# Performance work log

Hardware: AMD Instinct MI355X
Metric: run time of the kernel (lower is better)

Reference implementation:

```python
import jax, jax.numpy as jnp
import numpy as np

B, N = 256, 4096
IMG_W, IMG_H = 640.0, 480.0


def setup_inputs() -> dict:
    key = jax.random.key(0)
    k0, k1, k2, k3 = jax.random.split(key, 4)
    kpts0 = jax.random.uniform(k0, (B, N, 2), dtype=jnp.float32) * jnp.array([IMG_W, IMG_H], jnp.float32)
    kpts1 = jax.random.uniform(k1, (B, N, 2), dtype=jnp.float32) * jnp.array([IMG_W, IMG_H], jnp.float32)
    conf = jax.random.uniform(k2, (B, N, 1), dtype=jnp.float32)
    t_scale = jax.random.uniform(k3, (B, 2), dtype=jnp.float32) + 0.5
    Kmat = jnp.array([[500.0, 0.0, 320.0], [0.0, 500.0, 240.0], [0.0, 0.0, 1.0]], jnp.float32)
    K = jnp.tile(Kmat[None, None], (B, 2, 1, 1))
    gt_pose_0to1 = jnp.tile(jnp.eye(4, dtype=jnp.float32)[None], (B, 1, 1))
    return {"kpts0": kpts0, "kpts1": kpts1, "conf": conf, "t_scale": t_scale, "K": K, "gt_pose_0to1": gt_pose_0to1}


def _normalize(kpts, Kmat):
    # pixel -> normalized camera coords, homogeneous. kpts:[B,N,2], Kmat:[B,3,3] -> [B,N,3]
    Kinv = jnp.linalg.inv(Kmat)
    h = jnp.concatenate([kpts, jnp.ones_like(kpts[..., :1])], axis=-1)
    return jnp.einsum('bij,bnj->bni', Kinv, h)


def _se3_weighted_8pt(kpts0, kpts1, K0, K1, w, t_scale):
    b_, n_ = kpts0.shape[0], kpts0.shape[1]
    x0 = _normalize(kpts0, K0)  # [B,N,3]
    x1 = _normalize(kpts1, K1)  # [B,N,3]
    # epipolar constraint x1^T E x0 = 0 -> row kron(x1, x0): [B,N,9]
    X = (x1[..., :, None] * x0[..., None, :]).reshape(b_, n_, 9)
    # confidence-weighted normal equations, 9x9 per batch
    M = jnp.einsum('bn,bni,bnj->bij', w, X, X)
    _, V = jnp.linalg.eigh(M)
    E = V[..., 0].reshape(b_, 3, 3)  # eigvec of smallest eigenvalue
    # project to essential manifold + decompose
    U, S, Vt = jnp.linalg.svd(E)
    W = jnp.array([[0.0, -1.0, 0.0], [1.0, 0.0, 0.0], [0.0, 0.0, 1.0]], E.dtype)
    R1 = U @ W @ Vt
    R2 = U @ W.T @ Vt
    R1 = R1 * jnp.sign(jnp.linalg.det(R1))[:, None, None]
    R2 = R2 * jnp.sign(jnp.linalg.det(R2))[:, None, None]
    t = U[..., 2]  # [B,3]
    Rc = jnp.stack([R1, R1, R2, R2], axis=1)   # [B,4,3,3]
    tc = jnp.stack([t, -t, t, -t], axis=1)     # [B,4,3]
    # cheirality: solve d0 * (R x0) - d1 * x1 = -t in least squares (2x2 closed form)
    a = jnp.einsum('bcij,bnj->bcni', Rc, x0)   # [B,4,N,3]
    bvec = x1[:, None]                          # [B,1,N,3]
    tt = tc[:, :, None, :]                      # [B,4,1,3]
    aa = jnp.sum(a * a, -1)
    bb = jnp.sum(bvec * bvec, -1)
    ab = jnp.sum(a * bvec, -1)
    at = jnp.sum(a * tt, -1)
    bt = jnp.sum(bvec * tt, -1)
    det = aa * bb - ab * ab + 1e-9
    d0 = (-at * bb + ab * bt) / det
    d1 = (aa * bt - ab * at) / det
    pos = ((d0 > 0) & (d1 > 0)).astype(w.dtype)
    score = jnp.sum(w[:, None] * pos, -1)       # [B,4]
    best = jnp.argmax(jax.lax.stop_gradient(score), axis=-1)
    oh = jax.nn.one_hot(best, 4, dtype=kpts0.dtype)
    R = jnp.einsum('bc,bcij->bij', oh, Rc)
    t_best = jnp.einsum('bc,bci->bi', oh, tc)
    t_sc = t_best * t_scale[:, None]            # scale unit translation
    top = jnp.concatenate([R, t_sc[..., None]], axis=-1)  # [B,3,4]
    bot = jnp.broadcast_to(jnp.array([0.0, 0.0, 0.0, 1.0], R.dtype), (b_, 1, 4))
    return jnp.concatenate([top, bot], axis=1)  # [B,4,4]


def _se3_inverse(T):
    R = T[:, :3, :3]
    t = T[:, :3, 3:]
    Rt = jnp.swapaxes(R, -1, -2)
    tin = -(Rt @ t)
    top = jnp.concatenate([Rt, tin], axis=-1)
    bot = jnp.broadcast_to(jnp.array([0.0, 0.0, 0.0, 1.0], T.dtype), (T.shape[0], 1, 4))
    return jnp.concatenate([top, bot], axis=1)


def reference(kpts0, kpts1, conf, t_scale, K, gt_pose_0to1):
    w = conf[..., 0]
    T01 = _se3_weighted_8pt(kpts0, kpts1, K[:, 0], K[:, 1], w, t_scale[:, 0])
    T10 = _se3_inverse(T01)
    return jnp.stack([T01, T10], axis=1)  # [B,2,4,4]
```

## Files before the change

### kernel.cpp

```cpp
#include <hip/hip_runtime.h>
#include <math.h>

#define NBATCH 256
#define NPTS   4096
#define NT     512
#define PPT    (NPTS / NT)
#define NWAVE  (NT / 64)

#define IDX(r,c)   ((r)*((r)+1)/2+(c))
#define UPIDX(r,c) ((r)*9 - ((r)*((r)-1))/2 + ((c)-(r)))

__device__ __forceinline__ void inv3x3f(const float* __restrict__ Km, float* Ki) {
  double a = Km[0], bb = Km[1], c = Km[2];
  double d = Km[3], e  = Km[4], f = Km[5];
  double g = Km[6], h  = Km[7], i = Km[8];
  double C00 =  e*i - f*h;
  double C01 = -(d*i - f*g);
  double C02 =  d*h - e*g;
  double det = a*C00 + bb*C01 + c*C02;
  double rd = 1.0/det;
  Ki[0] = (float)(C00*rd); Ki[1] = (float)(-(bb*i - c*h)*rd); Ki[2] = (float)( (bb*f - c*e)*rd);
  Ki[3] = (float)(C01*rd); Ki[4] = (float)( (a*i  - c*g)*rd); Ki[5] = (float)(-(a*f  - c*d)*rd);
  Ki[6] = (float)(C02*rd); Ki[7] = (float)(-(a*h - bb*g)*rd); Ki[8] = (float)( (a*e  - bb*d)*rd);
}

__global__ __launch_bounds__(NT, 1)
void pose_fused(const float* __restrict__ kpts0,
                const float* __restrict__ kpts1,
                const float* __restrict__ conf,
                const float* __restrict__ t_scale,
                const float* __restrict__ Kmat,
                float* __restrict__ out)
{
  const int b    = blockIdx.x;
  const int tid  = threadIdx.x;
  const int lane = tid & 63;
  const int wv   = tid >> 6;

  __shared__ float  red[NWAVE][45];
  __shared__ double sMd[45];
  __shared__ double sLp[45];
  __shared__ double sDinv[9];
  __shared__ double sW[81];
  __shared__ double sB[81];
  __shared__ float  sR[21];
  __shared__ float  sscore[NWAVE][4];

  float Ki0[9], Ki1[9];
  inv3x3f(Kmat + (size_t)b*18,     Ki0);
  inv3x3f(Kmat + (size_t)b*18 + 9, Ki1);

  const float4* k0p4 = (const float4*)(kpts0 + (size_t)b*NPTS*2);
  const float4* k1p4 = (const float4*)(kpts1 + (size_t)b*NPTS*2);
  const float2* cp2  = (const float2*)(conf  + (size_t)b*NPTS);

  float px0[PPT][3], px1[PPT][3], pw[PPT];
  float acc[45];
#pragma unroll
  for (int j=0;j<45;j++) acc[j] = 0.f;

#pragma unroll
  for (int p=0;p<PPT/2;p++) {
    const int idx = tid + p*NT;
    const float4 q0 = k0p4[idx];
    const float4 q1 = k1p4[idx];
    const float2 w2 = cp2[idx];
#pragma unroll
    for (int h=0; h<2; h++) {
      const int pt = 2*p + h;
      const float u0 = h ? q0.z : q0.x, v0 = h ? q0.w : q0.y;
      const float u1 = h ? q1.z : q1.x, v1 = h ? q1.w : q1.y;
      const float w  = h ? w2.y : w2.x;
      float x0[3], x1[3];
      x0[0] = fmaf(Ki0[0],u0, fmaf(Ki0[1],v0, Ki0[2]));
      x0[1] = fmaf(Ki0[3],u0, fmaf(Ki0[4],v0, Ki0[5]));
      x0[2] = fmaf(Ki0[6],u0, fmaf(Ki0[7],v0, Ki0[8]));
      x1[0] = fmaf(Ki1[0],u1, fmaf(Ki1[1],v1, Ki1[2]));
      x1[1] = fmaf(Ki1[3],u1, fmaf(Ki1[4],v1, Ki1[5]));
      x1[2] = fmaf(Ki1[6],u1, fmaf(Ki1[7],v1, Ki1[8]));
#pragma unroll
      for (int j=0;j<3;j++) { px0[pt][j] = x0[j]; px1[pt][j] = x1[j]; }
      pw[pt] = w;
      float X[9], wX[9];
#pragma unroll
      for (int ii=0; ii<3; ii++)
#pragma unroll
        for (int jj=0; jj<3; jj++)
          X[ii*3+jj] = x1[ii]*x0[jj];
#pragma unroll
      for (int j=0;j<9;j++) wX[j] = w*X[j];
      int k = 0;
#pragma unroll
      for (int r=0;r<9;r++)
#pragma unroll
        for (int c=r;c<9;c++) { acc[k] = fmaf(wX[r], X[c], acc[k]); k++; }
    }
  }

#pragma unroll
  for (int j=0;j<45;j++) {
    float v = acc[j];
#pragma unroll
    for (int off=32; off>0; off>>=1) v += __shfl_xor(v, off, 64);
    acc[j] = v;
  }
  if (lane == 0) {
#pragma unroll
    for (int j=0;j<45;j++) red[wv][j] = acc[j];
  }
  __syncthreads();
  if (tid < 45) {
    double s = 0.0;
#pragma unroll
    for (int wq=0; wq<NWAVE; wq++) s += (double)red[wq][tid];
    sMd[tid] = s;
  }
  __syncthreads();

  if (wv == 0) {
    if (lane == 0) {
      double L[45];
#pragma unroll
      for (int r=0;r<9;r++)
#pragma unroll
        for (int c=0;c<=r;c++)
          L[IDX(r,c)] = sMd[UPIDX(c,r)];

      double dinv[9];
#pragma unroll
      for (int k=0;k<9;k++) {
        double s = L[IDX(k,k)];
#pragma unroll
        for (int j=0;j<k;j++) s -= L[IDX(k,j)]*L[IDX(k,j)];
        double l = sqrt(fmax(s, 1e-30));
        L[IDX(k,k)] = l;
        dinv[k] = 1.0/l;
#pragma unroll
        for (int i2=k+1;i2<9;i2++) {
          double s2 = L[IDX(i2,k)];
#pragma unroll
          for (int j=0;j<k;j++) s2 -= L[IDX(i2,j)]*L[IDX(k,j)];
          L[IDX(i2,k)] = s2*dinv[k];
        }
      }
#pragma unroll
      for (int j=0;j<45;j++) sLp[j] = L[j];
#pragma unroll
      for (int k=0;k<9;k++) sDinv[k] = dinv[k];
    }
    asm volatile("s_waitcnt lgkmcnt(0)" ::: "memory");
    __builtin_amdgcn_sched_barrier(0);

    double Brow[9];
    double vlan[9];
    if (lane < 9) {
      const double dj = sDinv[lane];
      double cw[9];
#pragma unroll
      for (int i=0;i<9;i++) cw[i] = (i == lane) ? dj : 0.0;
#pragma unroll
      for (int i2=1;i2<9;i2++) {
        double s = 0.0;
#pragma unroll
        for (int k=0;k<i2;k++) s = fma(sLp[IDX(i2,k)], cw[k], s);
        const double ci2 = -s*sDinv[i2];
        cw[i2] = (i2 > lane) ? ci2 : cw[i2];
      }
#pragma unroll
      for (int k=0;k<9;k++) sW[k*9 + lane] = cw[k];
    }
    asm volatile("s_waitcnt lgkmcnt(0)" ::: "memory");
    __builtin_amdgcn_sched_barrier(0);

    if (lane < 9) {
      double wcol[9];
#pragma unroll
      for (int k=0;k<9;k++) wcol[k] = sW[k*9 + lane];
#pragma unroll
      for (int j=0;j<9;j++) {
        double s = 0.0;
#pragma unroll
        for (int k=0;k<9;k++) s = fma(wcol[k], sW[k*9 + j], s);
        Brow[j] = s;
      }
#pragma unroll
      for (int j=0;j<9;j++) sB[lane*9 + j] = Brow[j];
    }
    asm volatile("s_waitcnt lgkmcnt(0)" ::: "memory");
    __builtin_amdgcn_sched_barrier(0);

    if (lane < 9) {
      double Crow[9];
#pragma unroll
      for (int j=0;j<9;j++) {
        double s = 0.0;
#pragma unroll
        for (int k=0;k<9;k++) s = fma(Brow[k], sB[k*9 + j], s);
        Crow[j] = s;
      }

      double vv[9];
#pragma unroll
      for (int j=0;j<9;j++) vv[j] = 0.125;
      vv[4] = 1.0;
      for (int it=0; it<10; ++it) {
        double p0 = fma(Crow[1], vv[1], Crow[0]*vv[0]);
        double p1 = fma(Crow[3], vv[3], Crow[2]*vv[2]);
        double p2 = fma(Crow[5], vv[5], Crow[4]*vv[4]);
        double p3 = fma(Crow[7], vv[7], Crow[6]*vv[6]);
        double p4 = Crow[8]*vv[8];
        double y  = ((p0 + p1) + (p2 + p3)) + p4;
#pragma unroll
        for (int j=0;j<9;j++) vv[j] = __shfl(y, j, 64);
      }
#pragma unroll
      for (int j=0;j<9;j++) vlan[j] = vv[j];
    }

    if (lane == 0) {
      double v[9];
#pragma unroll
      for (int j=0;j<9;j++) v[j] = vlan[j];
      {
        double nn = 0.0;
#pragma unroll
        for (int j=0;j<9;j++) nn += v[j]*v[j];
        double rn = 1.0/sqrt(nn);
#pragma unroll
        for (int j=0;j<9;j++) v[j] *= rn;
      }

      double E0[3][3];
#pragma unroll
      for (int ii=0;ii<3;ii++)
#pragma unroll
        for (int jj=0;jj<3;jj++) E0[ii][jj] = v[ii*3+jj];
      double G[3][3];
#pragma unroll
      for (int a2=0;a2<3;a2++)
#pragma unroll
        for (int b2=0;b2<3;b2++)
          G[a2][b2] = E0[0][a2]*E0[0][b2] + E0[1][a2]*E0[1][b2] + E0[2][a2]*E0[2][b2];
      double Vv[3][3] = {{1,0,0},{0,1,0},{0,0,1}};
#define JROT(P,Q,RR) do { \
      double apq = G[P][Q]; \
      if (fabs(apq) > 1e-18*(fabs(G[P][P])+fabs(G[Q][Q]))) { \
        double app = G[P][P], aqq = G[Q][Q]; \
        double tau = (aqq - app) / (2.0*apq); \
        double tt = ((tau >= 0.0) ? 1.0 : -1.0) / (fabs(tau) + sqrt(1.0 + tau*tau)); \
        double cc_ = 1.0/sqrt(1.0 + tt*tt); \
        double ss_ = tt*cc_; \
        G[P][P] = app - tt*apq; \
        G[Q][Q] = aqq + tt*apq; \
        G[P][Q] = 0.0; G[Q][P] = 0.0; \
        double grp = G[RR][P], grq = G[RR][Q]; \
        G[RR][P] = cc_*grp - ss_*grq; G[P][RR] = G[RR][P]; \
        G[RR][Q] = ss_*grp + cc_*grq; G[Q][RR] = G[RR][Q]; \
        double v0p = Vv[0][P], v0q = Vv[0][Q]; \
        Vv[0][P] = cc_*v0p - ss_*v0q; Vv[0][Q] = ss_*v0p + cc_*v0q; \
        double v1p = Vv[1][P], v1q = Vv[1][Q]; \
        Vv[1][P] = cc_*v1p - ss_*v1q; Vv[1][Q] = ss_*v1p + cc_*v1q; \
        double v2p = Vv[2][P], v2q = Vv[2][Q]; \
        Vv[2][P] = cc_*v2p - ss_*v2q; Vv[2][Q] = ss_*v2p + cc_*v2q; \
      } } while(0)
      for (int sw=0; sw<6; sw++) { JROT(0,1,2); JROT(0,2,1); JROT(1,2,0); }
#undef JROT
      double lam[3] = {G[0][0], G[1][1], G[2][2]};
#define CSWAP(A_,B_) if (lam[A_] < lam[B_]) { \
      double tl = lam[A_]; lam[A_] = lam[B_]; lam[B_] = tl; \
      double t0_ = Vv[0][A_]; Vv[0][A_] = Vv[0][B_]; Vv[0][B_] = t0_; \
      double t1_ = Vv[1][A_]; Vv[1][A_] = Vv[1][B_]; Vv[1][B_] = t1_; \
      double t2_ = Vv[2][A_]; Vv[2][A_] = Vv[2][B_]; Vv[2][B_] = t2_; }
      CSWAP(0,1); CSWAP(0,2); CSWAP(1,2);
#undef CSWAP
      double u1[3], u2[3], u3[3];
#pragma unroll
      for (int i3=0;i3<3;i3++)
        u1[i3] = E0[i3][0]*Vv[0][0] + E0[i3][1]*Vv[1][0] + E0[i3][2]*Vv[2][0];
      double n1 = 1.0/sqrt(fmax(u1[0]*u1[0]+u1[1]*u1[1]+u1[2]*u1[2], 1e-300));
#pragma unroll
      for (int i3=0;i3<3;i3++) u1[i3] *= n1;
#pragma unroll
      for (int i3=0;i3<3;i3++)
        u2[i3] = E0[i3][0]*Vv[0][1] + E0[i3][1]*Vv[1][1] + E0[i3][2]*Vv[2][1];
      double d12 = u1[0]*u2[0]+u1[1]*u2[1]+u1[2]*u2[2];
#pragma unroll
      for (int i3=0;i3<3;i3++) u2[i3] -= d12*u1[i3];
      double n2 = 1.0/sqrt(fmax(u2[0]*u2[0]+u2[1]*u2[1]+u2[2]*u2[2], 1e-300));
#pragma unroll
      for (int i3=0;i3<3;i3++) u2[i3] *= n2;
      u3[0] = u1[1]*u2[2] - u1[2]*u2[1];
      u3[1] = u1[2]*u2[0] - u1[0]*u2[2];
      u3[2] = u1[0]*u2[1] - u1[1]*u2[0];
      double R1a[9], R2a[9];
#pragma unroll
      for (int i3=0;i3<3;i3++)
#pragma unroll
        for (int j3=0;j3<3;j3++) {
          double m  = u3[i3]*Vv[j3][2];
          double pA = u2[i3]*Vv[j3][0] - u1[i3]*Vv[j3][1];
          R1a[i3*3+j3] = pA + m;
          R2a[i3*3+j3] = m - pA;
        }
      double det1 = R1a[0]*(R1a[4]*R1a[8]-R1a[5]*R1a[7])
                  - R1a[1]*(R1a[3]*R1a[8]-R1a[5]*R1a[6])
                  + R1a[2]*(R1a[3]*R1a[7]-R1a[4]*R1a[6]);
      double det2 = R2a[0]*(R2a[4]*R2a[8]-R2a[5]*R2a[7])
                  - R2a[1]*(R2a[3]*R2a[8]-R2a[5]*R2a[6])
                  + R2a[2]*(R2a[3]*R2a[7]-R2a[4]*R2a[6]);
      double sg1 = (det1 < 0.0) ? -1.0 : 1.0;
      double sg2 = (det2 < 0.0) ? -1.0 : 1.0;
#pragma unroll
      for (int j3=0;j3<9;j3++) { sR[j3] = (float)(sg1*R1a[j3]); sR[9+j3] = (float)(sg2*R2a[j3]); }
      sR[18] = (float)u3[0]; sR[19] = (float)u3[1]; sR[20] = (float)u3[2];
    }
  }
  __syncthreads();

  float r1[9], r2[9], tv[3];
#pragma unroll
  for (int j=0;j<9;j++) { r1[j] = sR[j]; r2[j] = sR[9+j]; }
  tv[0] = sR[18]; tv[1] = sR[19]; tv[2] = sR[20];

  float sc[4] = {0.f, 0.f, 0.f, 0.f};
#pragma unroll
  for (int p=0;p<PPT;p++) {
    const float x00 = px0[p][0], x01 = px0[p][1], x02 = px0[p][2];
    const float x10 = px1[p][0], x11 = px1[p][1], x12 = px1[p][2];
    const float w   = pw[p];
    const float bb2 = x10*x10 + x11*x11 + x12*x12;
    const float bt  = x10*tv[0] + x11*tv[1] + x12*tv[2];
    {
      float a0 = r1[0]*x00 + r1[1]*x01 + r1[2]*x02;
      float a1 = r1[3]*x00 + r1[4]*x01 + r1[5]*x02;
      float a2 = r1[6]*x00 + r1[7]*x01 + r1[8]*x02;
      float aa = a0*a0 + a1*a1 + a2*a2;
      float ab = a0*x10 + a1*x11 + a2*x12;
      float at = a0*tv[0] + a1*tv[1] + a2*tv[2];
      float n0v = ab*bt - at*bb2;
      float n1v = aa*bt - ab*at;
      if (n0v > 0.f && n1v > 0.f) sc[0] += w;
      if (n0v < 0.f && n1v < 0.f) sc[1] += w;
    }
    {
      float a0 = r2[0]*x00 + r2[1]*x01 + r2[2]*x02;
      float a1 = r2[3]*x00 + r2[4]*x01 + r2[5]*x02;
      float a2 = r2[6]*x00 + r2[7]*x01 + r2[8]*x02;
      float aa = a0*a0 + a1*a1 + a2*a2;
      float ab = a0*x10 + a1*x11 + a2*x12;
      float at = a0*tv[0] + a1*tv[1] + a2*tv[2];
      float n0v = ab*bt - at*bb2;
      float n1v = aa*bt - ab*at;
      if (n0v > 0.f && n1v > 0.f) sc[2] += w;
      if (n0v < 0.f && n1v < 0.f) sc[3] += w;
    }
  }
#pragma unroll
  for (int c=0;c<4;c++) {
    float vv = sc[c];
#pragma unroll
    for (int off=32; off>0; off>>=1) vv += __shfl_xor(vv, off, 64);
    sc[c] = vv;
  }
  if (lane == 0) {
#pragma unroll
    for (int c=0;c<4;c++) sscore[wv][c] = sc[c];
  }
  __syncthreads();

  if (tid == 0) {
    float st[4];
#pragma unroll
    for (int c=0;c<4;c++) {
      float s = 0.f;
#pragma unroll
      for (int wq=0; wq<NWAVE; wq++) s += sscore[wq][c];
      st[c] = s;
    }
    int bestc = 0; float bs = st[0];
    if (st[1] > bs) { bs = st[1]; bestc = 1; }
    if (st[2] > bs) { bs = st[2]; bestc = 2; }
    if (st[3] > bs) { bs = st[3]; bestc = 3; }
    float Rb[9];
#pragma unroll
    for (int j=0;j<9;j++) Rb[j] = (bestc < 2) ? r1[j] : r2[j];
    const float sg = (bestc & 1) ? -1.f : 1.f;
    const float ts = t_scale[(size_t)b*2];
    const float t0 = sg*tv[0]*ts, t1 = sg*tv[1]*ts, t2 = sg*tv[2]*ts;
    float* o = out + (size_t)b*32;
    o[0]=Rb[0]; o[1]=Rb[1]; o[2] =Rb[2]; o[3] =t0;
    o[4]=Rb[3]; o[5]=Rb[4]; o[6] =Rb[5]; o[7] =t1;
    o[8]=Rb[6]; o[9]=Rb[7]; o[10]=Rb[8]; o[11]=t2;
    o[12]=0.f; o[13]=0.f; o[14]=0.f; o[15]=1.f;
    const float ti0 = -(Rb[0]*t0 + Rb[3]*t1 + Rb[6]*t2);
    const float ti1 = -(Rb[1]*t0 + Rb[4]*t1 + Rb[7]*t2);
    const float ti2 = -(Rb[2]*t0 + Rb[5]*t1 + Rb[8]*t2);
    o[16]=Rb[0]; o[17]=Rb[3]; o[18]=Rb[6]; o[19]=ti0;
    o[20]=Rb[1]; o[21]=Rb[4]; o[22]=Rb[7]; o[23]=ti1;
    o[24]=Rb[2]; o[25]=Rb[5]; o[26]=Rb[8]; o[27]=ti2;
    o[28]=0.f; o[29]=0.f; o[30]=0.f; o[31]=1.f;
  }
}

extern "C" void kernel_launch(void* const* d_in, const int* in_sizes, int n_in,
                              void* d_out, int out_size, void* d_ws, size_t ws_size,
                              hipStream_t stream) {
  (void)in_sizes; (void)n_in; (void)out_size; (void)d_ws; (void)ws_size;
  const float* kpts0  = (const float*)d_in[0];
  const float* kpts1  = (const float*)d_in[1];
  const float* conf   = (const float*)d_in[2];
  const float* tscale = (const float*)d_in[3];
  const float* K      = (const float*)d_in[4];
  float* outp = (float*)d_out;
  pose_fused<<<dim3(NBATCH), dim3(NT), 0, stream>>>(kpts0, kpts1, conf, tscale, K, outp);
}
```

Baseline: 94.45 us.

## Use LDL^T factorization, square inverse once more, halve power iterations, drop normalization

Replaces the Cholesky factorization with a sqrt-free LDL^T form, folding the diagonal scaling into the inverse-product step. Adds one more squaring of the inverse matrix so power iteration runs 5 steps on M^-8 instead of 10 on M^-4. Moves the cross-wave reduction into wave 0 to remove a block barrier, and drops the eigenvector normalization, presumably because later steps are scale-invariant. This trims serial single-lane latency in the solve tail but risks overflow or scaling issues from the unnormalized higher matrix power.

New measurement: 92.72 us. No clear change (-1.8%).

```diff
diff --git a/kernel.cpp b/kernel.cpp
--- a/kernel.cpp
+++ b/kernel.cpp
@@ -43,6 +43,7 @@
   __shared__ double sDinv[9];
   __shared__ double sW[81];
   __shared__ double sB[81];
+  __shared__ double sC[81];
   __shared__ float  sR[21];
   __shared__ float  sscore[NWAVE][4];
 
@@ -109,15 +110,17 @@
     for (int j=0;j<45;j++) red[wv][j] = acc[j];
   }
   __syncthreads();
-  if (tid < 45) {
-    double s = 0.0;
-#pragma unroll
-    for (int wq=0; wq<NWAVE; wq++) s += (double)red[wq][tid];
-    sMd[tid] = s;
-  }
-  __syncthreads();
 
   if (wv == 0) {
+    if (lane < 45) {
+      double s = 0.0;
+#pragma unroll
+      for (int wq=0; wq<NWAVE; wq++) s += (double)red[wq][lane];
+      sMd[lane] = s;
+    }
+    asm volatile("s_waitcnt lgkmcnt(0)" ::: "memory");
+    __builtin_amdgcn_sched_barrier(0);
+
     if (lane == 0) {
       double L[45];
 #pragma unroll
@@ -126,22 +129,27 @@
         for (int c=0;c<=r;c++)
           L[IDX(r,c)] = sMd[UPIDX(c,r)];
 
-      double dinv[9];
+      double dv[9], dinv[9];
 #pragma unroll
       for (int k=0;k<9;k++) {
         double s = L[IDX(k,k)];
 #pragma unroll
-        for (int j=0;j<k;j++) s -= L[IDX(k,j)]*L[IDX(k,j)];
-        double l = sqrt(fmax(s, 1e-30));
-        L[IDX(k,k)] = l;
-        dinv[k] = 1.0/l;
+        for (int j=0;j<k;j++) {
+          double t = dv[j]*L[IDX(k,j)];
+          s -= t*L[IDX(k,j)];
+        }
+        s = fmax(s, 1e-30);
+        dv[k] = s;
+        const double di = 1.0/s;
+        dinv[k] = di;
 #pragma unroll
         for (int i2=k+1;i2<9;i2++) {
           double s2 = L[IDX(i2,k)];
 #pragma unroll
-          for (int j=0;j<k;j++) s2 -= L[IDX(i2,j)]*L[IDX(k,j)];
-          L[IDX(i2,k)] = s2*dinv[k];
+          for (int j=0;j<k;j++) s2 -= L[IDX(i2,j)]*(dv[j]*L[IDX(k,j)]);
+          L[IDX(i2,k)] = s2*di;
         }
+        L[IDX(k,k)] = s;
       }
 #pragma unroll
       for (int j=0;j<45;j++) sLp[j] = L[j];
@@ -152,19 +160,18 @@
     __builtin_amdgcn_sched_barrier(0);
 
     double Brow[9];
+    double Crow[9];
     double vlan[9];
     if (lane < 9) {
-      const double dj = sDinv[lane];
       double cw[9];
 #pragma unroll
-      for (int i=0;i<9;i++) cw[i] = (i == lane) ? dj : 0.0;
+      for (int i=0;i<9;i++) cw[i] = (i == lane) ? 1.0 : 0.0;
 #pragma unroll
       for (int i2=1;i2<9;i2++) {
         double s = 0.0;
 #pragma unroll
         for (int k=0;k<i2;k++) s = fma(sLp[IDX(i2,k)], cw[k], s);
-        const double ci2 = -s*sDinv[i2];
-        cw[i2] = (i2 > lane) ? ci2 : cw[i2];
+        cw[i2] = (i2 > lane) ? -s : cw[i2];
       }
 #pragma unroll
       for (int k=0;k<9;k++) sW[k*9 + lane] = cw[k];
@@ -175,7 +182,7 @@
     if (lane < 9) {
       double wcol[9];
 #pragma unroll
-      for (int k=0;k<9;k++) wcol[k] = sW[k*9 + lane];
+      for (int k=0;k<9;k++) wcol[k] = sW[k*9 + lane]*sDinv[k];
 #pragma unroll
       for (int j=0;j<9;j++) {
         double s = 0.0;
@@ -190,7 +197,6 @@
     __builtin_amdgcn_sched_barrier(0);
 
     if (lane < 9) {
-      double Crow[9];
 #pragma unroll
       for (int j=0;j<9;j++) {
         double s = 0.0;
@@ -198,17 +204,32 @@
         for (int k=0;k<9;k++) s = fma(Brow[k], sB[k*9 + j], s);
         Crow[j] = s;
       }
+#pragma unroll
+      for (int j=0;j<9;j++) sC[lane*9 + j] = Crow[j];
+    }
+    asm volatile("s_waitcnt lgkmcnt(0)" ::: "memory");
+    __builtin_amdgcn_sched_barrier(0);
+
+    if (lane < 9) {
+      double Drow[9];
+#pragma unroll
+      for (int j=0;j<9;j++) {
+        double s = 0.0;
+#pragma unroll
+        for (int k=0;k<9;k++) s = fma(Crow[k], sC[k*9 + j], s);
+        Drow[j] = s;
+      }
 
       double vv[9];
 #pragma unroll
       for (int j=0;j<9;j++) vv[j] = 0.125;
       vv[4] = 1.0;
-      for (int it=0; it<10; ++it) {
-        double p0 = fma(Crow[1], vv[1], Crow[0]*vv[0]);
-        double p1 = fma(Crow[3], vv[3], Crow[2]*vv[2]);
-        double p2 = fma(Crow[5], vv[5], Crow[4]*vv[4]);
-        double p3 = fma(Crow[7], vv[7], Crow[6]*vv[6]);
-        double p4 = Crow[8]*vv[8];
+      for (int it=0; it<5; ++it) {
+        double p0 = fma(Drow[1], vv[1], Drow[0]*vv[0]);
+        double p1 = fma(Drow[3], vv[3], Drow[2]*vv[2]);
+        double p2 = fma(Drow[5], vv[5], Drow[4]*vv[4]);
+        double p3 = fma(Drow[7], vv[7], Drow[6]*vv[6]);
+        double p4 = Drow[8]*vv[8];
         double y  = ((p0 + p1) + (p2 + p3)) + p4;
 #pragma unroll
         for (int j=0;j<9;j++) vv[j] = __shfl(y, j, 64);
@@ -221,14 +242,6 @@
       double v[9];
 #pragma unroll
       for (int j=0;j<9;j++) v[j] = vlan[j];
-      {
-        double nn = 0.0;
-#pragma unroll
-        for (int j=0;j<9;j++) nn += v[j]*v[j];
-        double rn = 1.0/sqrt(nn);
-#pragma unroll
-        for (int j=0;j<9;j++) v[j] *= rn;
-      }
 
       double E0[3][3];
 #pragma unroll
```
